# Kernel optimization log

Hardware: AMD Instinct MI355X
Metric: run time of the kernel (lower is better)

The kernel has to match this reference:

```python
import jax, jax.numpy as jnp
import numpy as np

B, S, D, H, L, DFF, WIN = 2, 2048, 768, 12, 2, 3072, 512
EPS = 1e-5
DH = D // H


def setup_inputs() -> dict:
    key = jax.random.key(0)
    ks = jax.random.split(key, 8)
    rn = lambda k, shape: jax.random.normal(k, shape, jnp.float32) * 0.02
    inp = {
        "src": jax.random.normal(ks[0], (B, S, D), jnp.float32),
        "qw": rn(ks[1], (L, D, D)), "qb": jnp.zeros((L, D), jnp.float32),
        "kw": rn(ks[2], (L, D, D)), "kb": jnp.zeros((L, D), jnp.float32),
        "vw": rn(ks[3], (L, D, D)), "vb": jnp.zeros((L, D), jnp.float32),
        "ow": rn(ks[4], (L, D, D)), "ob": jnp.zeros((L, D), jnp.float32),
        "w1": rn(ks[5], (L, DFF, D)), "b1": jnp.zeros((L, DFF), jnp.float32),
        "w2": rn(ks[6], (L, D, DFF)), "b2": jnp.zeros((L, D), jnp.float32),
        "g1": jnp.ones((L, D), jnp.float32), "be1": jnp.zeros((L, D), jnp.float32),
        "g2": jnp.ones((L, D), jnp.float32), "be2": jnp.zeros((L, D), jnp.float32),
    }
    return inp


def _ln(x, g, b):
    m = jnp.mean(x, axis=-1, keepdims=True)
    v = jnp.mean(jnp.square(x - m), axis=-1, keepdims=True)
    return (x - m) * jax.lax.rsqrt(v + EPS) * g + b


def _encoder(src, qw, qb, kw, kb, vw, vb, ow, ob, w1, b1, w2, b2, g1, be1, g2, be2):
    scale = DH ** -0.5
    idx = jnp.arange(S)
    # non-causal sliding window: |i - j| <= window_size // 2
    band = jnp.abs(idx[:, None] - idx[None, :]) <= (WIN // 2)
    neg = -jnp.finfo(jnp.float32).max
    x = src
    for l in range(L):
        # projections -> (B, H, S, DH)
        q = (x @ qw[l].T + qb[l]).reshape(B, S, H, DH).transpose(0, 2, 1, 3)
        k = (x @ kw[l].T + kb[l]).reshape(B, S, H, DH).transpose(0, 2, 1, 3)
        v = (x @ vw[l].T + vb[l]).reshape(B, S, H, DH).transpose(0, 2, 1, 3)
        # full dense scores then band mask (faithful to the original module)
        sim = jnp.einsum('bhid,bhjd->bhij', q * scale, k)
        sim = jnp.where(band, sim, neg)
        attn = jax.nn.softmax(sim, axis=-1)
        o = jnp.einsum('bhij,bhjd->bhid', attn, v)
        o = o.transpose(0, 2, 1, 3).reshape(B, S, D) @ ow[l].T + ob[l]
        # post-norm transformer block (norm_first=False)
        x = _ln(x + o, g1[l], be1[l])
        ff = jax.nn.relu(x @ w1[l].T + b1[l]) @ w2[l].T + b2[l]
        x = _ln(x + ff, g2[l], be2[l])
    return x


def reference(src, qw, qb, kw, kb, vw, vb, ow, ob, w1, b1, w2, b2, g1, be1, g2, be2):
    return _encoder(src, qw, qb, kw, kb, vw, vb, ow, ob, w1, b1, w2, b2, g1, be1, g2, be2)
```

## Files before the change

kernel.cpp:

```cpp
#include <hip/hip_runtime.h>
#include <math.h>

#define BATCH 2
#define SEQ   2048
#define DM    768
#define NHD   12
#define NL    2
#define DFF   3072
#define DH    64
#define HW    256
#define MR    (BATCH*SEQ)
#define EPSF  1e-5f
#define SCALE 0.125f
#define QKVS  2304

typedef __attribute__((ext_vector_type(8))) __bf16 bf16x8;
typedef __attribute__((ext_vector_type(4))) float  f32x4;

__device__ __forceinline__ ushort f2bu(float f) {
    union { __bf16 h; ushort u; } c;
    c.h = (__bf16)f;
    return c.u;
}
__device__ __forceinline__ float bu2f(ushort u) {
    union { uint u; float f; } c;
    c.u = ((uint)u) << 16;
    return c.f;
}

__device__ __forceinline__ void gload16(const ushort* g, ushort* l) {
    __builtin_amdgcn_global_load_lds(
        (const __attribute__((address_space(1))) void*)g,
        (__attribute__((address_space(3))) void*)l, 16, 0, 0);
}

__global__ __launch_bounds__(256) void cvt(const float* __restrict__ in,
                                           ushort* __restrict__ out, int n)
{
    int i = (blockIdx.x * 256 + threadIdx.x) * 4;
    if (i >= n) return;
    float4 v = *(const float4*)(in + i);
    ushort4 o;
    o.x = f2bu(v.x); o.y = f2bu(v.y); o.z = f2bu(v.z); o.w = f2bu(v.w);
    *(ushort4*)(out + i) = o;
}

__global__ __launch_bounds__(256) void gemm128(
    const ushort* __restrict__ A, const ushort* __restrict__ W,
    const float* __restrict__ bias, ushort* __restrict__ C,
    int M, int N, int K, int relu)
{
    __shared__ ushort As[128 * 32];
    __shared__ ushort Ws[128 * 32];

    const int t  = threadIdx.x;
    const int bm = blockIdx.y * 128;
    const int bn = blockIdx.x * 128;

    const int w    = t >> 6;
    const int lane = t & 63;
    const int quad = lane >> 4;
    const int lrow = lane & 15;
    const int wm   = (w >> 1) * 64;
    const int wn   = (w & 1) * 64;

    const int srow = t >> 2;
    const int scol = (t & 3) * 8;
    const ushort* ag = A + (size_t)(bm + srow) * K + scol;
    const ushort* wg = W + (size_t)(bn + srow) * K + scol;
    ushort* la0 = &As[t * 8];
    ushort* la1 = &As[2048 + t * 8];
    ushort* lw0 = &Ws[t * 8];
    ushort* lw1 = &Ws[2048 + t * 8];

    f32x4 acc[4][4] = {};

    for (int k0 = 0; k0 < K; k0 += 32) {
        gload16(ag + k0,                  la0);
        gload16(ag + (size_t)64 * K + k0, la1);
        gload16(wg + k0,                  lw0);
        gload16(wg + (size_t)64 * K + k0, lw1);
        __syncthreads();

        bf16x8 af[4], bfr[4];
#pragma unroll
        for (int i = 0; i < 4; ++i)
            af[i] = *(const bf16x8*)&As[(wm + i * 16 + lrow) * 32 + quad * 8];
#pragma unroll
        for (int j = 0; j < 4; ++j)
            bfr[j] = *(const bf16x8*)&Ws[(wn + j * 16 + lrow) * 32 + quad * 8];

#pragma unroll
        for (int i = 0; i < 4; ++i)
#pragma unroll
            for (int j = 0; j < 4; ++j)
                acc[i][j] = __builtin_amdgcn_mfma_f32_16x16x32_bf16(
                    af[i], bfr[j], acc[i][j], 0, 0, 0);
        __syncthreads();
    }

#pragma unroll
    for (int j = 0; j < 4; ++j) {
        const int col = bn + wn + j * 16 + lrow;
        const float bv = bias[col];
#pragma unroll
        for (int i = 0; i < 4; ++i) {
            const int rb = bm + wm + i * 16 + quad * 4;
#pragma unroll
            for (int r = 0; r < 4; ++r) {
                float vv = acc[i][j][r] + bv;
                if (relu) vv = fmaxf(vv, 0.f);
                C[(size_t)(rb + r) * N + col] = f2bu(vv);
            }
        }
    }
}

__global__ __launch_bounds__(256) void gemm64(
    const ushort* __restrict__ A, const ushort* __restrict__ W,
    const float* __restrict__ bias, ushort* __restrict__ C,
    float* __restrict__ part, int M, int N, int Kc, int ldk, int relu)
{
    __shared__ ushort As[64 * 32];
    __shared__ ushort Ws[128 * 32];

    const int t  = threadIdx.x;
    const int bm = blockIdx.y * 64;
    const int bn = blockIdx.x * 128;
    const int z  = blockIdx.z;
    const int kbase = z * Kc;

    const int w    = t >> 6;
    const int lane = t & 63;
    const int quad = lane >> 4;
    const int lrow = lane & 15;
    const int wm   = (w >> 1) * 32;
    const int wn   = (w & 1) * 64;

    const int srow = t >> 2;
    const int scol = (t & 3) * 8;
    const ushort* ag = A + (size_t)(bm + srow) * ldk + kbase + scol;
    const ushort* wg = W + (size_t)(bn + srow) * ldk + kbase + scol;
    ushort* la0 = &As[t * 8];
    ushort* lw0 = &Ws[t * 8];
    ushort* lw1 = &Ws[2048 + t * 8];

    f32x4 acc[2][4] = {};

    for (int k0 = 0; k0 < Kc; k0 += 32) {
        gload16(ag + k0,                    la0);
        gload16(wg + k0,                    lw0);
        gload16(wg + (size_t)64 * ldk + k0, lw1);
        __syncthreads();

        bf16x8 af[2], bfr[4];
#pragma unroll
        for (int i = 0; i < 2; ++i)
            af[i] = *(const bf16x8*)&As[(wm + i * 16 + lrow) * 32 + quad * 8];
#pragma unroll
        for (int j = 0; j < 4; ++j)
            bfr[j] = *(const bf16x8*)&Ws[(wn + j * 16 + lrow) * 32 + quad * 8];

#pragma unroll
        for (int i = 0; i < 2; ++i)
#pragma unroll
            for (int j = 0; j < 4; ++j)
                acc[i][j] = __builtin_amdgcn_mfma_f32_16x16x32_bf16(
                    af[i], bfr[j], acc[i][j], 0, 0, 0);
        __syncthreads();
    }

    if (gridDim.z > 1) {
        float* po = part + (size_t)z * M * N;
#pragma unroll
        for (int j = 0; j < 4; ++j) {
            const int col = bn + wn + j * 16 + lrow;
#pragma unroll
            for (int i = 0; i < 2; ++i) {
                const int rb = bm + wm + i * 16 + quad * 4;
#pragma unroll
                for (int r = 0; r < 4; ++r)
                    po[(size_t)(rb + r) * N + col] = acc[i][j][r];
            }
        }
    } else {
#pragma unroll
        for (int j = 0; j < 4; ++j) {
            const int col = bn + wn + j * 16 + lrow;
            const float bv = bias[col];
#pragma unroll
            for (int i = 0; i < 2; ++i) {
                const int rb = bm + wm + i * 16 + quad * 4;
#pragma unroll
                for (int r = 0; r < 4; ++r) {
                    float vv = acc[i][j][r] + bv;
                    if (relu) vv = fmaxf(vv, 0.f);
                    C[(size_t)(rb + r) * N + col] = f2bu(vv);
                }
            }
        }
    }
}

__global__ __launch_bounds__(256) void red_sk(
    const float* __restrict__ p, const float* __restrict__ bias,
    ushort* __restrict__ out)
{
    const int i = (blockIdx.x * 256 + threadIdx.x) * 4;
    float4 a = *(const float4*)(p + i);
    float4 b = *(const float4*)(p + (size_t)MR * DM + i);
    const int col = i % DM;
    float4 bv = *(const float4*)(bias + col);
    ushort4 o;
    o.x = f2bu(a.x + b.x + bv.x);
    o.y = f2bu(a.y + b.y + bv.y);
    o.z = f2bu(a.z + b.z + bv.z);
    o.w = f2bu(a.w + b.w + bv.w);
    *(ushort4*)(out + i) = o;
}

#define QT  64
#define NCH 9
#define KP  72

__global__ __launch_bounds__(256) void attn(
    const ushort* __restrict__ q, const ushort* __restrict__ k,
    const ushort* __restrict__ v, ushort* __restrict__ o)
{
    __shared__ ushort kv[64][KP];
    __shared__ ushort vt[64][KP];
    __shared__ ushort sc[QT][KP];

    const int t    = threadIdx.x;
    const int i0   = blockIdx.x * QT;
    const int h    = blockIdx.y;
    const int b    = blockIdx.z;
    const size_t ibase = (size_t)b * SEQ * QKVS + (size_t)h * DH;
    const size_t obase = (size_t)b * SEQ * DM   + (size_t)h * DH;

    const int w    = t >> 6;
    const int lane = t & 63;
    const int quad = lane >> 4;
    const int lrow = lane & 15;
    const int qrow = w * 16;

#pragma unroll
    for (int e = 0; e < 2; ++e) {
        int idx = t + 256 * e;
        int qi = idx >> 3, d0 = (idx & 7) * 8;
        uint4 raw = *(const uint4*)(q + ibase + (size_t)(i0 + qi) * QKVS + d0);
        *(uint4*)&sc[qi][d0] = raw;
    }
    __syncthreads();

    const bf16x8 a0 = *(const bf16x8*)&sc[qrow + lrow][quad * 8];
    const bf16x8 a1 = *(const bf16x8*)&sc[qrow + lrow][32 + quad * 8];

    float m_r[4], l_r[4];
    f32x4 oacc[4] = {};
#pragma unroll
    for (int r = 0; r < 4; ++r) { m_r[r] = -1e20f; l_r[r] = 0.f; }

    const int jstart = i0 - HW;

    for (int c = 0; c < NCH; ++c) {
        const int j0 = jstart + c * 64;

#pragma unroll
        for (int e = 0; e < 2; ++e) {
            int idx = t + 256 * e;
            int jj = idx >> 3, d0 = (idx & 7) * 8;
            int j = j0 + jj;
            uint4 kr = make_uint4(0, 0, 0, 0);
            uint4 vr = make_uint4(0, 0, 0, 0);
            if (j >= 0 && j < SEQ) {
                kr = *(const uint4*)(k + ibase + (size_t)j * QKVS + d0);
                vr = *(const uint4*)(v + ibase + (size_t)j * QKVS + d0);
            }
            *(uint4*)&kv[jj][d0] = kr;
            const ushort* u = (const ushort*)&vr;
#pragma unroll
            for (int x = 0; x < 8; ++x) {
                int dh  = d0 + x;
                int blk = ((jj >> 3) ^ (dh >> 3)) & 7;
                vt[dh][blk * 8 + (jj & 7)] = u[x];
            }
        }
        __syncthreads();

        float p[4][4];
#pragma unroll
        for (int kt = 0; kt < 4; ++kt) {
            const int krow = kt * 16;
            bf16x8 b0 = *(const bf16x8*)&kv[krow + lrow][quad * 8];
            bf16x8 b1 = *(const bf16x8*)&kv[krow + lrow][32 + quad * 8];
            f32x4 acc = {};
            acc = __builtin_amdgcn_mfma_f32_16x16x32_bf16(a0, b0, acc, 0, 0, 0);
            acc = __builtin_amdgcn_mfma_f32_16x16x32_bf16(a1, b1, acc, 0, 0, 0);
            const int jg = j0 + krow + lrow;
#pragma unroll
            for (int r = 0; r < 4; ++r) {
                const int ig = i0 + qrow + quad * 4 + r;
                bool ok = (jg >= 0) && (jg < SEQ) &&
                          (jg >= ig - HW) && (jg <= ig + HW);
                p[kt][r] = ok ? acc[r] * SCALE : -1e30f;
            }
        }

#pragma unroll
        for (int r = 0; r < 4; ++r) {
            float cm = fmaxf(fmaxf(p[0][r], p[1][r]), fmaxf(p[2][r], p[3][r]));
#pragma unroll
            for (int off = 8; off; off >>= 1) cm = fmaxf(cm, __shfl_xor(cm, off));
            const float mn = fmaxf(m_r[r], cm);
            const float f  = __expf(m_r[r] - mn);
            m_r[r] = mn;
            float cs = 0.f;
#pragma unroll
            for (int kt = 0; kt < 4; ++kt) {
                float e = __expf(p[kt][r] - mn);
                p[kt][r] = e;
                cs += e;
            }
#pragma unroll
            for (int off = 8; off; off >>= 1) cs += __shfl_xor(cs, off);
            l_r[r] = l_r[r] * f + cs;
#pragma unroll
            for (int nt = 0; nt < 4; ++nt) oacc[nt][r] *= f;
        }

#pragma unroll
        for (int kt = 0; kt < 4; ++kt)
#pragma unroll
            for (int r = 0; r < 4; ++r)
                sc[qrow + quad * 4 + r][kt * 16 + lrow] = f2bu(p[kt][r]);

        bf16x8 pa0 = *(const bf16x8*)&sc[qrow + lrow][quad * 8];
        bf16x8 pa1 = *(const bf16x8*)&sc[qrow + lrow][32 + quad * 8];
#pragma unroll
        for (int nt = 0; nt < 4; ++nt) {
            const int dh  = nt * 16 + lrow;
            const int rsw = (dh >> 3) & 7;
            bf16x8 b0 = *(const bf16x8*)&vt[dh][((quad)     ^ rsw) * 8];
            bf16x8 b1 = *(const bf16x8*)&vt[dh][((quad + 4) ^ rsw) * 8];
            oacc[nt] = __builtin_amdgcn_mfma_f32_16x16x32_bf16(pa0, b0, oacc[nt], 0, 0, 0);
            oacc[nt] = __builtin_amdgcn_mfma_f32_16x16x32_bf16(pa1, b1, oacc[nt], 0, 0, 0);
        }
        __syncthreads();
    }

#pragma unroll
    for (int r = 0; r < 4; ++r) {
        const float inv = 1.f / l_r[r];
        const int qi = i0 + qrow + quad * 4 + r;
#pragma unroll
        for (int nt = 0; nt < 4; ++nt)
            o[obase + (size_t)qi * DM + nt * 16 + lrow] = f2bu(oacc[nt][r] * inv);
    }
}

__global__ __launch_bounds__(64) void add_ln(
    const ushort* __restrict__ xa, const ushort* __restrict__ yb,
    const float* __restrict__ g, const float* __restrict__ be,
    ushort* __restrict__ ob, float* __restrict__ of, int fin)
{
    const int r = blockIdx.x, t = threadIdx.x;
    const size_t off = (size_t)r * DM;
    float sv[12];
    float s1 = 0.f, s2 = 0.f;
#pragma unroll
    for (int ii = 0; ii < 12; ++ii) {
        float vv = bu2f(xa[off + t + 64 * ii]) + bu2f(yb[off + t + 64 * ii]);
        sv[ii] = vv; s1 += vv; s2 += vv * vv;
    }
#pragma unroll
    for (int o2 = 32; o2; o2 >>= 1) {
        s1 += __shfl_xor(s1, o2);
        s2 += __shfl_xor(s2, o2);
    }
    const float mean = s1 * (1.f / 768.f);
    const float rstd = rsqrtf(s2 * (1.f / 768.f) - mean * mean + EPSF);
#pragma unroll
    for (int ii = 0; ii < 12; ++ii) {
        const int c = t + 64 * ii;
        float v = (sv[ii] - mean) * rstd * g[c] + be[c];
        if (fin) of[off + c] = v;
        else     ob[off + c] = f2bu(v);
    }
}

extern "C" void kernel_launch(void* const* d_in, const int* in_sizes, int n_in,
                              void* d_out, int out_size, void* d_ws, size_t ws_size,
                              hipStream_t stream) {
    (void)in_sizes; (void)n_in; (void)out_size; (void)ws_size;
    const float* src = (const float*)d_in[0];
    const float* qw  = (const float*)d_in[1];
    const float* qb  = (const float*)d_in[2];
    const float* kw  = (const float*)d_in[3];
    const float* kb  = (const float*)d_in[4];
    const float* vw  = (const float*)d_in[5];
    const float* vb  = (const float*)d_in[6];
    const float* ow  = (const float*)d_in[7];
    const float* ob  = (const float*)d_in[8];
    const float* w1  = (const float*)d_in[9];
    const float* b1  = (const float*)d_in[10];
    const float* w2  = (const float*)d_in[11];
    const float* b2  = (const float*)d_in[12];
    const float* g1  = (const float*)d_in[13];
    const float* be1 = (const float*)d_in[14];
    const float* g2  = (const float*)d_in[15];
    const float* be2 = (const float*)d_in[16];

    const size_t A    = (size_t)MR * DM;
    const size_t WD1  = (size_t)DM * DM;
    const size_t WQKV = (size_t)3 * DM * DM;
    const size_t WF1  = (size_t)DFF * DM;
    const size_t WF   = (size_t)NL * WF1;

    float*  bcat = (float*)d_ws;
    ushort* p    = (ushort*)(bcat + (size_t)NL * QKVS);
    ushort* qkvwB = p; p += (size_t)NL * WQKV;
    ushort* owB   = p; p += (size_t)NL * WD1;
    ushort* w1B   = p; p += WF;
    ushort* w2B   = p; p += WF;
    ushort* xb    = p; p += A;
    ushort* qkvB  = p; p += 3 * A;
    ushort* oB    = p; p += A;
    ushort* yB    = p; p += A;
    ushort* h1    = p; p += A;
    ushort* ffh   = p;

    float* part = (float*)qkvB;

    for (int l = 0; l < NL; ++l) {
        hipMemcpyAsync(bcat + (size_t)l * QKVS + 0,    qb + (size_t)l * DM,
                       DM * sizeof(float), hipMemcpyDeviceToDevice, stream);
        hipMemcpyAsync(bcat + (size_t)l * QKVS + DM,   kb + (size_t)l * DM,
                       DM * sizeof(float), hipMemcpyDeviceToDevice, stream);
        hipMemcpyAsync(bcat + (size_t)l * QKVS + 2*DM, vb + (size_t)l * DM,
                       DM * sizeof(float), hipMemcpyDeviceToDevice, stream);
    }

    for (int l = 0; l < NL; ++l) {
        cvt<<<(int)(WD1 / 1024), 256, 0, stream>>>(
            qw + (size_t)l * WD1, qkvwB + (size_t)l * WQKV + 0,     (int)WD1);
        cvt<<<(int)(WD1 / 1024), 256, 0, stream>>>(
            kw + (size_t)l * WD1, qkvwB + (size_t)l * WQKV + WD1,   (int)WD1);
        cvt<<<(int)(WD1 / 1024), 256, 0, stream>>>(
            vw + (size_t)l * WD1, qkvwB + (size_t)l * WQKV + 2*WD1, (int)WD1);
    }
    cvt<<<(int)(NL * WD1 / 1024), 256, 0, stream>>>(ow, owB, (int)(NL * WD1));
    cvt<<<(int)(WF / 1024), 256, 0, stream>>>(w1, w1B, (int)WF);
    cvt<<<(int)(WF / 1024), 256, 0, stream>>>(w2, w2B, (int)WF);
    cvt<<<(int)(A  / 1024), 256, 0, stream>>>(src, xb, (int)A);

    const dim3 gQKV(QKVS / 128, MR / 128);
    const dim3 gO(DM / 128, MR / 64);
    const dim3 gF1(DFF / 128, MR / 128);
    const dim3 gF2(DM / 128, MR / 64, 2);
    const dim3 gA(SEQ / QT, NHD, BATCH);

    for (int l = 0; l < NL; ++l) {
        const size_t bD = (size_t)l * DM;
        const size_t bF = (size_t)l * DFF;

        gemm128<<<gQKV, 256, 0, stream>>>(xb, qkvwB + (size_t)l * WQKV,
                                          bcat + (size_t)l * QKVS, qkvB,
                                          MR, QKVS, DM, 0);
        attn<<<gA, 256, 0, stream>>>(qkvB, qkvB + DM, qkvB + 2 * DM, oB);
        gemm64<<<gO, 256, 0, stream>>>(oB, owB + (size_t)l * WD1, ob + bD, yB,
                                       nullptr, MR, DM, DM, DM, 0);
        add_ln<<<MR, 64, 0, stream>>>(xb, yB, g1 + bD, be1 + bD,
                                      h1, nullptr, 0);
        gemm128<<<gF1, 256, 0, stream>>>(h1, w1B + (size_t)l * WF1, b1 + bF, ffh,
                                         MR, DFF, DM, 1);
        gemm64<<<gF2, 256, 0, stream>>>(ffh, w2B + (size_t)l * WF1, nullptr,
                                        nullptr, part, MR, DM, DFF / 2, DFF, 0);
        red_sk<<<(int)(A / 1024), 256, 0, stream>>>(part, b2 + bD, xb);
        if (l == NL - 1)
            add_ln<<<MR, 64, 0, stream>>>(h1, xb, g2 + bD, be2 + bD,
                                          nullptr, (float*)d_out, 1);
        else
            add_ln<<<MR, 64, 0, stream>>>(h1, xb, g2 + bD, be2 + bD,
                                          xb, nullptr, 0);
    }
}
```

Before: 513.3 us.

## Double-buffer attention K/V tiles, swizzle blocks across XCDs, batch LayerNorm rows

The attention kernel now prefetches the next K/V chunk into registers while computing on the current one. It stores that chunk into a second LDS buffer, leaving one barrier per chunk instead of a load-then-sync stall. GEMM and attention kernels remap block indices so consecutive work groups land on the same XCD, aiming for better L2 reuse. add_ln now processes four rows per 256-thread block instead of one row per 64-thread block, cutting block count. Costs are doubled LDS for K/V and more registers in the attention kernel.

```diff
diff --git a/kernel.cpp b/kernel.cpp
--- a/kernel.cpp
+++ b/kernel.cpp
@@ -34,6 +34,17 @@
         (__attribute__((address_space(3))) void*)l, 16, 0, 0);
 }
 
+__device__ __forceinline__ void xcd_swz(int& bx, int& by, int& bz) {
+    const int gx = gridDim.x, gy = gridDim.y;
+    const int nwg = gx * gy * gridDim.z;
+    int lin = bx + gx * (by + gy * bz);
+    lin = (lin & 7) * (nwg >> 3) + (lin >> 3);
+    bx = lin % gx;
+    int rest = lin / gx;
+    by = rest % gy;
+    bz = rest / gy;
+}
+
 __global__ __launch_bounds__(256) void cvt(const float* __restrict__ in,
                                            ushort* __restrict__ out, int n)
 {
@@ -53,9 +64,12 @@
     __shared__ ushort As[128 * 32];
     __shared__ ushort Ws[128 * 32];
 
+    int bxi = blockIdx.x, byi = blockIdx.y, bzi = blockIdx.z;
+    xcd_swz(bxi, byi, bzi);
+
     const int t  = threadIdx.x;
-    const int bm = blockIdx.y * 128;
-    const int bn = blockIdx.x * 128;
+    const int bm = byi * 128;
+    const int bn = bxi * 128;
 
     const int w    = t >> 6;
     const int lane = t & 63;
@@ -124,10 +138,13 @@
     __shared__ ushort As[64 * 32];
     __shared__ ushort Ws[128 * 32];
 
+    int bxi = blockIdx.x, byi = blockIdx.y, bzi = blockIdx.z;
+    xcd_swz(bxi, byi, bzi);
+
     const int t  = threadIdx.x;
-    const int bm = blockIdx.y * 64;
-    const int bn = blockIdx.x * 128;
-    const int z  = blockIdx.z;
+    const int bm = byi * 64;
+    const int bn = bxi * 128;
+    const int z  = bzi;
     const int kbase = z * Kc;
 
     const int w    = t >> 6;
@@ -227,14 +244,17 @@
     const ushort* __restrict__ q, const ushort* __restrict__ k,
     const ushort* __restrict__ v, ushort* __restrict__ o)
 {
-    __shared__ ushort kv[64][KP];
-    __shared__ ushort vt[64][KP];
+    __shared__ ushort kv[2][64][KP];
+    __shared__ ushort vt[2][64][KP];
     __shared__ ushort sc[QT][KP];
 
+    int bxi = blockIdx.x, byi = blockIdx.y, bzi = blockIdx.z;
+    xcd_swz(bxi, byi, bzi);
+
     const int t    = threadIdx.x;
-    const int i0   = blockIdx.x * QT;
-    const int h    = blockIdx.y;
-    const int b    = blockIdx.z;
+    const int i0   = bxi * QT;
+    const int h    = byi;
+    const int b    = bzi;
     const size_t ibase = (size_t)b * SEQ * QKVS + (size_t)h * DH;
     const size_t obase = (size_t)b * SEQ * DM   + (size_t)h * DH;
 
@@ -244,6 +264,11 @@
     const int lrow = lane & 15;
     const int qrow = w * 16;
 
+    const int jstart = i0 - HW;
+
+    const int sjj[2] = { t >> 3, (t + 256) >> 3 };
+    const int sd0[2] = { (t & 7) * 8, (t & 7) * 8 };
+
 #pragma unroll
     for (int e = 0; e < 2; ++e) {
         int idx = t + 256 * e;
@@ -251,6 +276,28 @@
         uint4 raw = *(const uint4*)(q + ibase + (size_t)(i0 + qi) * QKVS + d0);
         *(uint4*)&sc[qi][d0] = raw;
     }
+    uint4 kr[2], vr[2];
+#pragma unroll
+    for (int e = 0; e < 2; ++e) {
+        int j = jstart + sjj[e];
+        kr[e] = make_uint4(0, 0, 0, 0);
+        vr[e] = make_uint4(0, 0, 0, 0);
+        if (j >= 0 && j < SEQ) {
+            kr[e] = *(const uint4*)(k + ibase + (size_t)j * QKVS + sd0[e]);
+            vr[e] = *(const uint4*)(v + ibase + (size_t)j * QKVS + sd0[e]);
+        }
+    }
+#pragma unroll
+    for (int e = 0; e < 2; ++e) {
+        *(uint4*)&kv[0][sjj[e]][sd0[e]] = kr[e];
+        const ushort* u = (const ushort*)&vr[e];
+#pragma unroll
+        for (int x = 0; x < 8; ++x) {
+            int dh  = sd0[e] + x;
+            int blk = ((sjj[e] >> 3) ^ (dh >> 3)) & 7;
+            vt[0][dh][blk * 8 + (sjj[e] & 7)] = u[x];
+        }
+    }
     __syncthreads();
 
     const bf16x8 a0 = *(const bf16x8*)&sc[qrow + lrow][quad * 8];
@@ -261,39 +308,30 @@
 #pragma unroll
     for (int r = 0; r < 4; ++r) { m_r[r] = -1e20f; l_r[r] = 0.f; }
 
-    const int jstart = i0 - HW;
-
     for (int c = 0; c < NCH; ++c) {
-        const int j0 = jstart + c * 64;
-
-#pragma unroll
-        for (int e = 0; e < 2; ++e) {
-            int idx = t + 256 * e;
-            int jj = idx >> 3, d0 = (idx & 7) * 8;
-            int j = j0 + jj;
-            uint4 kr = make_uint4(0, 0, 0, 0);
-            uint4 vr = make_uint4(0, 0, 0, 0);
-            if (j >= 0 && j < SEQ) {
-                kr = *(const uint4*)(k + ibase + (size_t)j * QKVS + d0);
-                vr = *(const uint4*)(v + ibase + (size_t)j * QKVS + d0);
-            }
-            *(uint4*)&kv[jj][d0] = kr;
-            const ushort* u = (const ushort*)&vr;
-#pragma unroll
-            for (int x = 0; x < 8; ++x) {
-                int dh  = d0 + x;
-                int blk = ((jj >> 3) ^ (dh >> 3)) & 7;
-                vt[dh][blk * 8 + (jj & 7)] = u[x];
-            }
-        }
-        __syncthreads();
+        const int cur = c & 1;
+        const int j0  = jstart + c * 64;
+
+        if (c + 1 < NCH) {
+            const int j0n = jstart + (c + 1) * 64;
+#pragma unroll
+            for (int e = 0; e < 2; ++e) {
+                int j = j0n + sjj[e];
+                kr[e] = make_uint4(0, 0, 0, 0);
+                vr[e] = make_uint4(0, 0, 0, 0);
+                if (j >= 0 && j < SEQ) {
+                    kr[e] = *(const uint4*)(k + ibase + (size_t)j * QKVS + sd0[e]);
+                    vr[e] = *(const uint4*)(v + ibase + (size_t)j * QKVS + sd0[e]);
+                }
+            }
+        }
 
         float p[4][4];
 #pragma unroll
         for (int kt = 0; kt < 4; ++kt) {
             const int krow = kt * 16;
-            bf16x8 b0 = *(const bf16x8*)&kv[krow + lrow][quad * 8];
-            bf16x8 b1 = *(const bf16x8*)&kv[krow + lrow][32 + quad * 8];
+            bf16x8 b0 = *(const bf16x8*)&kv[cur][krow + lrow][quad * 8];
+            bf16x8 b1 = *(const bf16x8*)&kv[cur][krow + lrow][32 + quad * 8];
             f32x4 acc = {};
             acc = __builtin_amdgcn_mfma_f32_16x16x32_bf16(a0, b0, acc, 0, 0, 0);
             acc = __builtin_amdgcn_mfma_f32_16x16x32_bf16(a1, b1, acc, 0, 0, 0);
@@ -341,10 +379,25 @@
         for (int nt = 0; nt < 4; ++nt) {
             const int dh  = nt * 16 + lrow;
             const int rsw = (dh >> 3) & 7;
-            bf16x8 b0 = *(const bf16x8*)&vt[dh][((quad)     ^ rsw) * 8];
-            bf16x8 b1 = *(const bf16x8*)&vt[dh][((quad + 4) ^ rsw) * 8];
+            bf16x8 b0 = *(const bf16x8*)&vt[cur][dh][((quad)     ^ rsw) * 8];
+            bf16x8 b1 = *(const bf16x8*)&vt[cur][dh][((quad + 4) ^ rsw) * 8];
             oacc[nt] = __builtin_amdgcn_mfma_f32_16x16x32_bf16(pa0, b0, oacc[nt], 0, 0, 0);
             oacc[nt] = __builtin_amdgcn_mfma_f32_16x16x32_bf16(pa1, b1, oacc[nt], 0, 0, 0);
+        }
+
+        if (c + 1 < NCH) {
+            const int nxt = cur ^ 1;
+#pragma unroll
+            for (int e = 0; e < 2; ++e) {
+                *(uint4*)&kv[nxt][sjj[e]][sd0[e]] = kr[e];
+                const ushort* u = (const ushort*)&vr[e];
+#pragma unroll
+                for (int x = 0; x < 8; ++x) {
+                    int dh  = sd0[e] + x;
+                    int blk = ((sjj[e] >> 3) ^ (dh >> 3)) & 7;
+                    vt[nxt][dh][blk * 8 + (sjj[e] & 7)] = u[x];
+                }
+            }
         }
         __syncthreads();
     }
@@ -359,12 +412,13 @@
     }
 }
 
-__global__ __launch_bounds__(64) void add_ln(
+__global__ __launch_bounds__(256) void add_ln(
     const ushort* __restrict__ xa, const ushort* __restrict__ yb,
     const float* __restrict__ g, const float* __restrict__ be,
     ushort* __restrict__ ob, float* __restrict__ of, int fin)
 {
-    const int r = blockIdx.x, t = threadIdx.x;
+    const int r = blockIdx.x * 4 + (threadIdx.x >> 6);
+    const int t = threadIdx.x & 63;
     const size_t off = (size_t)r * DM;
     float sv[12];
     float s1 = 0.f, s2 = 0.f;
@@ -470,18 +524,18 @@
         attn<<<gA, 256, 0, stream>>>(qkvB, qkvB + DM, qkvB + 2 * DM, oB);
         gemm64<<<gO, 256, 0, stream>>>(oB, owB + (size_t)l * WD1, ob + bD, yB,
                                        nullptr, MR, DM, DM, DM, 0);
-        add_ln<<<MR, 64, 0, stream>>>(xb, yB, g1 + bD, be1 + bD,
-                                      h1, nullptr, 0);
+        add_ln<<<MR / 4, 256, 0, stream>>>(xb, yB, g1 + bD, be1 + bD,
+                                           h1, nullptr, 0);
         gemm128<<<gF1, 256, 0, stream>>>(h1, w1B + (size_t)l * WF1, b1 + bF, ffh,
                                          MR, DFF, DM, 1);
         gemm64<<<gF2, 256, 0, stream>>>(ffh, w2B + (size_t)l * WF1, nullptr,
                                         nullptr, part, MR, DM, DFF / 2, DFF, 0);
         red_sk<<<(int)(A / 1024), 256, 0, stream>>>(part, b2 + bD, xb);
         if (l == NL - 1)
-            add_ln<<<MR, 64, 0, stream>>>(h1, xb, g2 + bD, be2 + bD,
-                                          nullptr, (float*)d_out, 1);
+            add_ln<<<MR / 4, 256, 0, stream>>>(h1, xb, g2 + bD, be2 + bD,
+                                               nullptr, (float*)d_out, 1);
         else
-            add_ln<<<MR, 64, 0, stream>>>(h1, xb, g2 + bD, be2 + bD,
-                                          xb, nullptr, 0);
-    }
-}
+            add_ln<<<MR / 4, 256, 0, stream>>>(h1, xb, g2 + bD, be2 + bD,
+                                               xb, nullptr, 0);
+    }
+}
```

New measurement: 498.3 us. 1.03x faster.
